# Performance work log

Measured on AMD Instinct MI355X. Metric: run time of the kernel, lower is better.

The kernel has to match this reference:

```python
import jax, jax.numpy as jnp
import numpy as np

N = 100000        # nodes in the batched graph
E = 1_600_000     # directed edges
G = 256           # graphs in the batch
IN, H = 3, 64
EPS = 1e-5        # BatchNorm eps (eval mode: running stats, dropout off)


def setup_inputs() -> dict:
    key = jax.random.key(0)
    ks = jax.random.split(key, 40)
    inp = {}
    inp["x"] = jax.random.normal(ks[0], (N, IN), jnp.float32)
    inp["edge_index"] = jax.random.randint(ks[1], (2, E), 0, N, dtype=jnp.int32)
    inp["batch_idx"] = jnp.sort(jax.random.randint(ks[2], (N,), 0, G, dtype=jnp.int32))
    dims = [IN, H, H, H]  # zip(dims[:-1], dims[1:]) -> 3 GCN layers (as in source)
    k = 3
    for i in range(3):
        inp[f"W{i}"] = jax.random.normal(ks[k], (dims[i], dims[i + 1]), jnp.float32) * 0.1; k += 1
        inp[f"b{i}"] = jax.random.normal(ks[k], (dims[i + 1],), jnp.float32) * 0.01; k += 1
        inp[f"g{i}"] = jax.random.uniform(ks[k], (dims[i + 1],), jnp.float32, 0.5, 1.5); k += 1
        inp[f"be{i}"] = jax.random.normal(ks[k], (dims[i + 1],), jnp.float32) * 0.1; k += 1
        inp[f"rm{i}"] = jax.random.normal(ks[k], (dims[i + 1],), jnp.float32) * 0.1; k += 1
        inp[f"rv{i}"] = jax.random.uniform(ks[k], (dims[i + 1],), jnp.float32, 0.5, 1.5); k += 1
    inp["mW1"] = jax.random.normal(ks[k], (2 * H, 32), jnp.float32) * 0.1; k += 1
    inp["mb1"] = jnp.zeros((32,), jnp.float32)
    inp["mW2"] = jax.random.normal(ks[k], (32, 16), jnp.float32) * 0.1; k += 1
    inp["mb2"] = jnp.zeros((16,), jnp.float32)
    inp["mW3"] = jax.random.normal(ks[k], (16, 1), jnp.float32) * 0.1; k += 1
    inp["mb3"] = jnp.zeros((1,), jnp.float32)
    return inp


def _gcn(x, W, b, src, dst):
    # PyG GCNConv: add self-loops, symmetric D^-1/2 (A+I) D^-1/2 normalization
    h = x @ W                                   # [N, out]
    deg = jnp.zeros((N,), h.dtype).at[dst].add(1.0) + 1.0  # +1 self-loop
    dinv = jax.lax.rsqrt(deg)
    coef = dinv[src] * dinv[dst]                # [E]
    agg = jax.ops.segment_sum(h[src] * coef[:, None], dst, num_segments=N)
    agg = agg + h * (dinv * dinv)[:, None]      # self-loop message
    return agg + b


def _bn(x, g, be, rm, rv):
    return (x - rm) * jax.lax.rsqrt(rv + EPS) * g + be


def _forward(x, edge_index, batch_idx,
             W0, b0, g0, be0, rm0, rv0,
             W1, b1, g1, be1, rm1, rv1,
             W2, b2, g2, be2, rm2, rv2,
             mW1, mb1, mW2, mb2, mW3, mb3):
    src, dst = edge_index[0], edge_index[1]
    layers = [(W0, b0, g0, be0, rm0, rv0), (W1, b1, g1, be1, rm1, rv1), (W2, b2, g2, be2, rm2, rv2)]
    for (W, b, g, be, rm, rv) in layers:
        x = jax.nn.relu(_bn(_gcn(x, W, b, src, dst), g, be, rm, rv))
    cnt = jax.ops.segment_sum(jnp.ones((N,), x.dtype), batch_idx, num_segments=G)
    x_mean = jax.ops.segment_sum(x, batch_idx, num_segments=G) / jnp.maximum(cnt, 1.0)[:, None]
    x_max = jax.ops.segment_max(x, batch_idx, num_segments=G)
    x_max = jnp.where(jnp.isfinite(x_max), x_max, 0.0)
    xg = jnp.concatenate([x_mean, x_max], axis=1)  # [G, 2H]
    h = jax.nn.relu(xg @ mW1 + mb1)
    h = jax.nn.relu(h @ mW2 + mb2)
    return h @ mW3 + mb3                            # [G, 1]


def reference(x, edge_index, batch_idx,
              W0, b0, g0, be0, rm0, rv0,
              W1, b1, g1, be1, rm1, rv1,
              W2, b2, g2, be2, rm2, rv2,
              mW1, mb1, mW2, mb2, mW3, mb3):
    return _forward(x, edge_index, batch_idx,
                    W0, b0, g0, be0, rm0, rv0,
                    W1, b1, g1, be1, rm1, rv1,
                    W2, b2, g2, be2, rm2, rv2,
                    mW1, mb1, mW2, mb2, mW3, mb3)
```

## Files before the change

### kernel.cpp

```cpp
#include <hip/hip_runtime.h>
#include <hip/hip_fp16.h>

#define NN 100000
#define EE 1600000
#define GG 256
#define EPS 1e-5f
#define KB2 ((NN + 511) >> 9)
#define EPB 4096
#define EBLK ((EE + EPB - 1) / EPB)
#define NB256 ((NN + 255) / 256)

__device__ __forceinline__ unsigned int pack2(float x, float y) {
  __half2 h = __float22half2_rn(make_float2(x, y));
  return *reinterpret_cast<unsigned int*>(&h);
}
__device__ __forceinline__ uint2 pack4(float x, float y, float z, float w) {
  uint2 r;
  r.x = pack2(x, y);
  r.y = pack2(z, w);
  return r;
}
__device__ __forceinline__ void add4(float4& a, uint2 v) {
  __half2 h0 = *reinterpret_cast<__half2*>(&v.x);
  __half2 h1 = *reinterpret_cast<__half2*>(&v.y);
  float2 f0 = __half22float2(h0);
  float2 f1 = __half22float2(h1);
  a.x += f0.x; a.y += f0.y; a.z += f1.x; a.w += f1.y;
}

__global__ void k_bcnt(const int* __restrict__ ei, int* __restrict__ bcnt) {
  __shared__ int cnt[KB2];
  int t = threadIdx.x;
  for (int i = t; i < KB2; i += 256) cnt[i] = 0;
  __syncthreads();
  int e0 = blockIdx.x * EPB;
#pragma unroll
  for (int j = 0; j < 16; ++j) {
    int e = e0 + j * 256 + t;
    if (e < EE) atomicAdd(&cnt[ei[EE + e] >> 9], 1);
  }
  __syncthreads();
  for (int i = t; i < KB2; i += 256)
    if (cnt[i] > 0) atomicAdd(&bcnt[i], cnt[i]);
}

__global__ void k_bscan(const int* __restrict__ bcnt, int* __restrict__ bbase,
                        int* __restrict__ bfill, int* __restrict__ row) {
  __shared__ int s[256];
  int t = threadIdx.x;
  int v = (t < KB2) ? bcnt[t] : 0;
  s[t] = v;
  __syncthreads();
  for (int off = 1; off < 256; off <<= 1) {
    int add = (t >= off) ? s[t - off] : 0;
    __syncthreads();
    s[t] += add;
    __syncthreads();
  }
  if (t < KB2) {
    int e = s[t] - v;
    bbase[t] = e;
    bfill[t] = e;
  }
  if (t == 0) {
    bbase[KB2] = EE;
    row[NN] = EE;
  }
}

__global__ void k_passA(const int* __restrict__ ei, int* __restrict__ bfill,
                        int2* __restrict__ tmp) {
  __shared__ int cnt[KB2], cur[KB2], base[KB2];
  int t = threadIdx.x;
  for (int b = t; b < KB2; b += 256) { cnt[b] = 0; cur[b] = 0; }
  __syncthreads();
  int e0 = blockIdx.x * EPB;
  int myb[16];
#pragma unroll
  for (int j = 0; j < 16; ++j) {
    int e = e0 + j * 256 + t;
    int bb = -1;
    if (e < EE) bb = ei[EE + e] >> 9;
    myb[j] = bb;
    if (bb >= 0) atomicAdd(&cnt[bb], 1);
  }
  __syncthreads();
  for (int b = t; b < KB2; b += 256)
    if (cnt[b] > 0) base[b] = atomicAdd(&bfill[b], cnt[b]);
  __syncthreads();
#pragma unroll
  for (int j = 0; j < 16; ++j) {
    int e = e0 + j * 256 + t;
    int bb = myb[j];
    if (bb >= 0) {
      int slot = base[bb] + atomicAdd(&cur[bb], 1);
      tmp[slot] = make_int2(ei[e], ei[EE + e]);
    }
  }
}

__global__ void k_bucket(const int2* __restrict__ tmp, const int* __restrict__ bbase,
                         const float* __restrict__ x, int* __restrict__ csr,
                         int* __restrict__ row, float* __restrict__ dinv,
                         float4* __restrict__ xd) {
  __shared__ int cnt[512], s[512], fillp[512];
  int b = blockIdx.x, t = threadIdx.x;
  int nb = b << 9;
  int e0 = bbase[b], e1 = bbase[b + 1];
  cnt[t] = 0;
  cnt[t + 256] = 0;
  __syncthreads();
  for (int e = e0 + t; e < e1; e += 256) atomicAdd(&cnt[tmp[e].y & 511], 1);
  __syncthreads();
  s[t] = cnt[t];
  s[t + 256] = cnt[t + 256];
  __syncthreads();
  for (int off = 1; off < 512; off <<= 1) {
    int i1 = t + 256;
    int v0 = (t >= off) ? s[t - off] : 0;
    int v1 = (i1 >= off) ? s[i1 - off] : 0;
    __syncthreads();
    s[t] += v0;
    s[i1] += v1;
    __syncthreads();
  }
#pragma unroll
  for (int k = 0; k < 2; ++k) {
    int i = t + k * 256;
    int excl = s[i] - cnt[i];
    fillp[i] = excl;
    int dst = nb + i;
    if (dst < NN) {
      row[dst] = e0 + excl;
      float d = rsqrtf((float)cnt[i] + 1.0f);
      dinv[dst] = d;
      xd[dst] = make_float4(x[dst * 3] * d, x[dst * 3 + 1] * d, x[dst * 3 + 2] * d, 0.f);
    }
  }
  __syncthreads();
  for (int e = e0 + t; e < e1; e += 256) {
    int2 ed = tmp[e];
    int slot = atomicAdd(&fillp[ed.y & 511], 1);
    csr[e0 + slot] = ed.x;
  }
}

__global__ void k_agg3f(const float4* __restrict__ xd, const int* __restrict__ row,
                        const int* __restrict__ csr, const float* __restrict__ dinv,
                        const float* __restrict__ W, const float* __restrict__ b,
                        const float* __restrict__ gam, const float* __restrict__ bet,
                        const float* __restrict__ rm, const float* __restrict__ rv,
                        uint2* __restrict__ out) {
  int n = blockIdx.x * 256 + threadIdx.x;
  if (n >= NN) return;
  int s0 = row[n], s1 = row[n + 1];
  float4 a = xd[n];
  float ax = a.x, ay = a.y, az = a.z;
  for (int i = s0; i < s1; i += 16) {
    int rem = s1 - i;
    int idx[16];
#pragma unroll
    for (int j = 0; j < 16; ++j) idx[j] = csr[min(i + j, s1 - 1)];
    float4 v[16];
#pragma unroll
    for (int j = 0; j < 16; ++j) v[j] = xd[idx[j]];
#pragma unroll
    for (int j = 0; j < 16; ++j)
      if (j < rem) { ax += v[j].x; ay += v[j].y; az += v[j].z; }
  }
  float d = dinv[n];
  float t0 = ax * d, t1 = ay * d, t2 = az * d;
  const float4* W4 = (const float4*)W;
  const float4* b4 = (const float4*)b;
  const float4* g4p = (const float4*)gam;
  const float4* be4p = (const float4*)bet;
  const float4* rm4p = (const float4*)rm;
  const float4* rv4p = (const float4*)rv;
#pragma unroll
  for (int c4 = 0; c4 < 16; ++c4) {
    float4 w0 = W4[c4], w1 = W4[16 + c4], w2 = W4[32 + c4];
    float4 bb = b4[c4], g4 = g4p[c4], be4 = be4p[c4], rm4 = rm4p[c4], rv4 = rv4p[c4];
    float4 o;
    o.x = fmaf(t0, w0.x, fmaf(t1, w1.x, fmaf(t2, w2.x, bb.x)));
    o.y = fmaf(t0, w0.y, fmaf(t1, w1.y, fmaf(t2, w2.y, bb.y)));
    o.z = fmaf(t0, w0.z, fmaf(t1, w1.z, fmaf(t2, w2.z, bb.z)));
    o.w = fmaf(t0, w0.w, fmaf(t1, w1.w, fmaf(t2, w2.w, bb.w)));
    float scx = g4.x * rsqrtf(rv4.x + EPS), shx = be4.x - rm4.x * scx;
    float scy = g4.y * rsqrtf(rv4.y + EPS), shy = be4.y - rm4.y * scy;
    float scz = g4.z * rsqrtf(rv4.z + EPS), shz = be4.z - rm4.z * scz;
    float scw = g4.w * rsqrtf(rv4.w + EPS), shw = be4.w - rm4.w * scw;
    o.x = fmaxf(fmaf(o.x, scx, shx), 0.f) * d;
    o.y = fmaxf(fmaf(o.y, scy, shy), 0.f) * d;
    o.z = fmaxf(fmaf(o.z, scz, shz), 0.f) * d;
    o.w = fmaxf(fmaf(o.w, scw, shw), 0.f) * d;
    out[(size_t)n * 16 + c4] = pack4(o.x, o.y, o.z, o.w);
  }
}

template <bool MID>
__global__ void k_layer2(const uint2* __restrict__ xs, const int* __restrict__ row,
                         const int* __restrict__ csr, const float* __restrict__ dinv,
                         const float* __restrict__ W, const float* __restrict__ b,
                         const float* __restrict__ gam, const float* __restrict__ bet,
                         const float* __restrict__ rm, const float* __restrict__ rv,
                         void* __restrict__ outv) {
  __shared__ float sh[16][68];
  int t = blockIdx.x * 256 + threadIdx.x;
  int n = t >> 4, sub = t & 15;
  int local = threadIdx.x >> 4;
  if (n >= NN) return;
  int s0 = row[n], s1 = row[n + 1];
  float4 a = make_float4(0.f, 0.f, 0.f, 0.f);
  add4(a, xs[(size_t)n * 16 + sub]);
  if (s0 < s1) {
    int e = s0 + sub;
    int myidx = (e < s1) ? csr[e] : n;
    for (int i = s0; i < s1; i += 16) {
      int e2 = i + 16 + sub;
      int pre = csr[min(e2, s1 - 1)];
      int nidx = (e2 < s1) ? pre : n;
      int rem = s1 - i;
      uint2 v[16];
#pragma unroll
      for (int j = 0; j < 16; ++j) {
        int idx = __shfl(myidx, j, 16);
        v[j] = xs[(size_t)idx * 16 + sub];
      }
#pragma unroll
      for (int j = 0; j < 16; ++j)
        if (j < rem) add4(a, v[j]);
      myidx = nidx;
    }
  }
  float d = dinv[n];
  sh[local][sub * 4 + 0] = a.x * d;
  sh[local][sub * 4 + 1] = a.y * d;
  sh[local][sub * 4 + 2] = a.z * d;
  sh[local][sub * 4 + 3] = a.w * d;
  __syncthreads();
  const float4* W4 = (const float4*)W;
  float4 acc = ((const float4*)b)[sub];
#pragma unroll 8
  for (int k = 0; k < 64; ++k) {
    float xv = sh[local][k];
    float4 w = W4[k * 16 + sub];
    acc.x = fmaf(xv, w.x, acc.x);
    acc.y = fmaf(xv, w.y, acc.y);
    acc.z = fmaf(xv, w.z, acc.z);
    acc.w = fmaf(xv, w.w, acc.w);
  }
  float4 g4 = ((const float4*)gam)[sub];
  float4 be4 = ((const float4*)bet)[sub];
  float4 rm4 = ((const float4*)rm)[sub];
  float4 rv4 = ((const float4*)rv)[sub];
  float scx = g4.x * rsqrtf(rv4.x + EPS), shx = be4.x - rm4.x * scx;
  float scy = g4.y * rsqrtf(rv4.y + EPS), shy = be4.y - rm4.y * scy;
  float scz = g4.z * rsqrtf(rv4.z + EPS), shz = be4.z - rm4.z * scz;
  float scw = g4.w * rsqrtf(rv4.w + EPS), shw = be4.w - rm4.w * scw;
  float4 o;
  o.x = fmaxf(fmaf(acc.x, scx, shx), 0.f);
  o.y = fmaxf(fmaf(acc.y, scy, shy), 0.f);
  o.z = fmaxf(fmaf(acc.z, scz, shz), 0.f);
  o.w = fmaxf(fmaf(acc.w, scw, shw), 0.f);
  if (MID) {
    ((uint2*)outv)[(size_t)n * 16 + sub] = pack4(o.x * d, o.y * d, o.z * d, o.w * d);
  } else {
    ((float4*)outv)[(size_t)n * 16 + sub] = o;
  }
}

__device__ __forceinline__ int lower_bound(const int* __restrict__ b, int target) {
  int lo = 0, hi = NN;
  while (lo < hi) {
    int m = (lo + hi) >> 1;
    if (b[m] < target) lo = m + 1; else hi = m;
  }
  return lo;
}

__global__ void k_poolmlp(const float* __restrict__ feat, const int* __restrict__ bidx,
                          const float* __restrict__ mW1, const float* __restrict__ mb1,
                          const float* __restrict__ mW2, const float* __restrict__ mb2,
                          const float* __restrict__ mW3, const float* __restrict__ mb3,
                          float* __restrict__ out) {
  __shared__ float ssum[4][64], smax[4][64], xg[128], h1[32], h2[16];
  int g = blockIdx.x, t = threadIdx.x;
  int c = t & 63, q = t >> 6;
  int lo = lower_bound(bidx, g);
  int hi = lower_bound(bidx, g + 1);
  float s = 0.f, m = 0.f;
  for (int i = lo + q; i < hi; i += 4) {
    float v = feat[(size_t)i * 64 + c];
    s += v;
    m = fmaxf(m, v);
  }
  ssum[q][c] = s;
  smax[q][c] = m;
  __syncthreads();
  if (q == 0) {
    float cs = ssum[0][c] + ssum[1][c] + ssum[2][c] + ssum[3][c];
    float cm = fmaxf(fmaxf(smax[0][c], smax[1][c]), fmaxf(smax[2][c], smax[3][c]));
    float cnt = fmaxf((float)(hi - lo), 1.0f);
    xg[c] = cs / cnt;
    xg[64 + c] = cm;
  }
  __syncthreads();
  if (t < 32) {
    float a = mb1[t];
    for (int k = 0; k < 128; ++k) a = fmaf(xg[k], mW1[k * 32 + t], a);
    h1[t] = fmaxf(a, 0.f);
  }
  __syncthreads();
  if (t < 16) {
    float a = mb2[t];
    for (int k = 0; k < 32; ++k) a = fmaf(h1[k], mW2[k * 16 + t], a);
    h2[t] = fmaxf(a, 0.f);
  }
  __syncthreads();
  if (t == 0) {
    float a = mb3[0];
    for (int k = 0; k < 16; ++k) a = fmaf(h2[k], mW3[k], a);
    out[g] = a;
  }
}

extern "C" void kernel_launch(void* const* d_in, const int* in_sizes, int n_in,
                              void* d_out, int out_size, void* d_ws, size_t ws_size,
                              hipStream_t stream) {
  const float* x = (const float*)d_in[0];
  const int* ei = (const int*)d_in[1];
  const int* bidx = (const int*)d_in[2];
  const float *W[3], *b[3], *gam[3], *bet[3], *rm[3], *rv[3];
  for (int l = 0; l < 3; ++l) {
    W[l] = (const float*)d_in[3 + 6 * l];
    b[l] = (const float*)d_in[4 + 6 * l];
    gam[l] = (const float*)d_in[5 + 6 * l];
    bet[l] = (const float*)d_in[6 + 6 * l];
    rm[l] = (const float*)d_in[7 + 6 * l];
    rv[l] = (const float*)d_in[8 + 6 * l];
  }
  const float* mW1 = (const float*)d_in[21];
  const float* mb1 = (const float*)d_in[22];
  const float* mW2 = (const float*)d_in[23];
  const float* mb2 = (const float*)d_in[24];
  const float* mW3 = (const float*)d_in[25];
  const float* mb3 = (const float*)d_in[26];
  float* out = (float*)d_out;

  char* ws = (char*)d_ws;
  size_t off = 0;
  auto alloc = [&](size_t bytes) {
    void* p = ws + off;
    off = (off + bytes + 1023) & ~(size_t)1023;
    return p;
  };
  float* dinv = (float*)alloc(NN * 4);
  int* row = (int*)alloc((NN + 1) * 4);
  int* csr = (int*)alloc((size_t)EE * 4);
  int* bcnt = (int*)alloc(256 * 4);
  int* bbase = (int*)alloc(256 * 4);
  int* bfill = (int*)alloc(256 * 4);
  float4* xd = (float4*)alloc((size_t)NN * 16);
  float* bufA = (float*)alloc((size_t)NN * 64 * 4);
  float* bufB = (float*)alloc((size_t)NN * 64 * 4);
  int2* tmp = (int2*)bufA;

  hipMemsetAsync(bcnt, 0, 256 * 4, stream);

  k_bcnt<<<EBLK, 256, 0, stream>>>(ei, bcnt);
  k_bscan<<<1, 256, 0, stream>>>(bcnt, bbase, bfill, row);
  k_passA<<<EBLK, 256, 0, stream>>>(ei, bfill, tmp);
  k_bucket<<<KB2, 256, 0, stream>>>(tmp, bbase, x, csr, row, dinv, xd);

  int nb16 = (NN * 16 + 255) / 256;

  k_agg3f<<<NB256, 256, 0, stream>>>(xd, row, csr, dinv, W[0], b[0], gam[0], bet[0],
                                     rm[0], rv[0], (uint2*)bufA);
  k_layer2<true><<<nb16, 256, 0, stream>>>((const uint2*)bufA, row, csr, dinv, W[1], b[1],
                                           gam[1], bet[1], rm[1], rv[1], (void*)bufB);
  k_layer2<false><<<nb16, 256, 0, stream>>>((const uint2*)bufB, row, csr, dinv, W[2], b[2],
                                            gam[2], bet[2], rm[2], rv[2], (void*)bufA);
  k_poolmlp<<<GG, 256, 0, stream>>>(bufA, bidx, mW1, mb1, mW2, mb2, mW3, mb3, out);
}
```

Before: 380.6 us.

## Pack edge temp to one int, double-buffer layer gathers, vectorize pooling

The bucketing temp array now stores each edge as a single int, holding the source shifted left by 9 bits plus the low 9 bits of the destination, instead of an int2. This halves that scratch traffic in passA and the bucket kernel; the packing only works because node ids fit in 23 bits. The layer2 gather loop is restructured to issue the next 16 neighbor loads before accumulating the current batch, which holds more loads in flight at the cost of registers. Pooling reads float4 per thread across 16 rows with a shared-memory reduction, replacing scalar loads over 4 rows.

```diff
diff --git a/kernel.cpp b/kernel.cpp
--- a/kernel.cpp
+++ b/kernel.cpp
@@ -69,7 +69,7 @@
 }
 
 __global__ void k_passA(const int* __restrict__ ei, int* __restrict__ bfill,
-                        int2* __restrict__ tmp) {
+                        int* __restrict__ tmp) {
   __shared__ int cnt[KB2], cur[KB2], base[KB2];
   int t = threadIdx.x;
   for (int b = t; b < KB2; b += 256) { cnt[b] = 0; cur[b] = 0; }
@@ -94,12 +94,12 @@
     int bb = myb[j];
     if (bb >= 0) {
       int slot = base[bb] + atomicAdd(&cur[bb], 1);
-      tmp[slot] = make_int2(ei[e], ei[EE + e]);
+      tmp[slot] = (ei[e] << 9) | (ei[EE + e] & 511);
     }
   }
 }
 
-__global__ void k_bucket(const int2* __restrict__ tmp, const int* __restrict__ bbase,
+__global__ void k_bucket(const int* __restrict__ tmp, const int* __restrict__ bbase,
                          const float* __restrict__ x, int* __restrict__ csr,
                          int* __restrict__ row, float* __restrict__ dinv,
                          float4* __restrict__ xd) {
@@ -110,7 +110,7 @@
   cnt[t] = 0;
   cnt[t + 256] = 0;
   __syncthreads();
-  for (int e = e0 + t; e < e1; e += 256) atomicAdd(&cnt[tmp[e].y & 511], 1);
+  for (int e = e0 + t; e < e1; e += 256) atomicAdd(&cnt[tmp[e] & 511], 1);
   __syncthreads();
   s[t] = cnt[t];
   s[t + 256] = cnt[t + 256];
@@ -139,9 +139,9 @@
   }
   __syncthreads();
   for (int e = e0 + t; e < e1; e += 256) {
-    int2 ed = tmp[e];
-    int slot = atomicAdd(&fillp[ed.y & 511], 1);
-    csr[e0 + slot] = ed.x;
+    int ed = tmp[e];
+    int slot = atomicAdd(&fillp[ed & 511], 1);
+    csr[e0 + slot] = ed >> 9;
   }
 }
 
@@ -213,23 +213,38 @@
   float4 a = make_float4(0.f, 0.f, 0.f, 0.f);
   add4(a, xs[(size_t)n * 16 + sub]);
   if (s0 < s1) {
-    int e = s0 + sub;
-    int myidx = (e < s1) ? csr[e] : n;
-    for (int i = s0; i < s1; i += 16) {
-      int e2 = i + 16 + sub;
-      int pre = csr[min(e2, s1 - 1)];
-      int nidx = (e2 < s1) ? pre : n;
-      int rem = s1 - i;
-      uint2 v[16];
-#pragma unroll
-      for (int j = 0; j < 16; ++j) {
-        int idx = __shfl(myidx, j, 16);
-        v[j] = xs[(size_t)idx * 16 + sub];
+    int pre0 = csr[min(s0 + sub, s1 - 1)];
+    int myidx = (s0 + sub < s1) ? pre0 : n;
+    uint2 vA[16];
+#pragma unroll
+    for (int j = 0; j < 16; ++j) {
+      int idx = __shfl(myidx, j, 16);
+      vA[j] = xs[(size_t)idx * 16 + sub];
+    }
+    int i = s0;
+    while (true) {
+      int inext = i + 16;
+      if (inext < s1) {
+        int pre = csr[min(inext + sub, s1 - 1)];
+        int nidx = (inext + sub < s1) ? pre : n;
+        uint2 vB[16];
+#pragma unroll
+        for (int j = 0; j < 16; ++j) {
+          int idx = __shfl(nidx, j, 16);
+          vB[j] = xs[(size_t)idx * 16 + sub];
+        }
+#pragma unroll
+        for (int j = 0; j < 16; ++j) add4(a, vA[j]);
+#pragma unroll
+        for (int j = 0; j < 16; ++j) vA[j] = vB[j];
+        i = inext;
+      } else {
+        int rem = s1 - i;
+#pragma unroll
+        for (int j = 0; j < 16; ++j)
+          if (j < rem) add4(a, vA[j]);
+        break;
       }
-#pragma unroll
-      for (int j = 0; j < 16; ++j)
-        if (j < rem) add4(a, v[j]);
-      myidx = nidx;
     }
   }
   float d = dinv[n];
@@ -278,31 +293,42 @@
   return lo;
 }
 
-__global__ void k_poolmlp(const float* __restrict__ feat, const int* __restrict__ bidx,
+__global__ void k_poolmlp(const float4* __restrict__ feat, const int* __restrict__ bidx,
                           const float* __restrict__ mW1, const float* __restrict__ mb1,
                           const float* __restrict__ mW2, const float* __restrict__ mb2,
                           const float* __restrict__ mW3, const float* __restrict__ mb3,
                           float* __restrict__ out) {
-  __shared__ float ssum[4][64], smax[4][64], xg[128], h1[32], h2[16];
+  __shared__ float4 shs[16][17], shm[16][17];
+  __shared__ float xg[128], h1[32], h2[16];
   int g = blockIdx.x, t = threadIdx.x;
-  int c = t & 63, q = t >> 6;
+  int c4 = t & 15, r = t >> 4;
   int lo = lower_bound(bidx, g);
   int hi = lower_bound(bidx, g + 1);
-  float s = 0.f, m = 0.f;
-  for (int i = lo + q; i < hi; i += 4) {
-    float v = feat[(size_t)i * 64 + c];
-    s += v;
-    m = fmaxf(m, v);
-  }
-  ssum[q][c] = s;
-  smax[q][c] = m;
-  __syncthreads();
-  if (q == 0) {
-    float cs = ssum[0][c] + ssum[1][c] + ssum[2][c] + ssum[3][c];
-    float cm = fmaxf(fmaxf(smax[0][c], smax[1][c]), fmaxf(smax[2][c], smax[3][c]));
-    float cnt = fmaxf((float)(hi - lo), 1.0f);
-    xg[c] = cs / cnt;
-    xg[64 + c] = cm;
+  float4 s = make_float4(0.f, 0.f, 0.f, 0.f);
+  float4 m = make_float4(0.f, 0.f, 0.f, 0.f);
+  for (int i = lo + r; i < hi; i += 16) {
+    float4 v = feat[(size_t)i * 16 + c4];
+    s.x += v.x; s.y += v.y; s.z += v.z; s.w += v.w;
+    m.x = fmaxf(m.x, v.x); m.y = fmaxf(m.y, v.y);
+    m.z = fmaxf(m.z, v.z); m.w = fmaxf(m.w, v.w);
+  }
+  shs[r][c4] = s;
+  shm[r][c4] = m;
+  __syncthreads();
+  if (t < 16) {
+    float4 cs = shs[0][t], cm = shm[0][t];
+#pragma unroll
+    for (int r2 = 1; r2 < 16; ++r2) {
+      float4 as = shs[r2][t], am = shm[r2][t];
+      cs.x += as.x; cs.y += as.y; cs.z += as.z; cs.w += as.w;
+      cm.x = fmaxf(cm.x, am.x); cm.y = fmaxf(cm.y, am.y);
+      cm.z = fmaxf(cm.z, am.z); cm.w = fmaxf(cm.w, am.w);
+    }
+    float inv = 1.0f / fmaxf((float)(hi - lo), 1.0f);
+    xg[t * 4 + 0] = cs.x * inv; xg[t * 4 + 1] = cs.y * inv;
+    xg[t * 4 + 2] = cs.z * inv; xg[t * 4 + 3] = cs.w * inv;
+    xg[64 + t * 4 + 0] = cm.x; xg[64 + t * 4 + 1] = cm.y;
+    xg[64 + t * 4 + 2] = cm.z; xg[64 + t * 4 + 3] = cm.w;
   }
   __syncthreads();
   if (t < 32) {
@@ -363,7 +389,7 @@
   float4* xd = (float4*)alloc((size_t)NN * 16);
   float* bufA = (float*)alloc((size_t)NN * 64 * 4);
   float* bufB = (float*)alloc((size_t)NN * 64 * 4);
-  int2* tmp = (int2*)bufA;
+  int* tmp = (int*)bufA;
 
   hipMemsetAsync(bcnt, 0, 256 * 4, stream);
 
@@ -380,5 +406,5 @@
                                            gam[1], bet[1], rm[1], rv[1], (void*)bufB);
   k_layer2<false><<<nb16, 256, 0, stream>>>((const uint2*)bufB, row, csr, dinv, W[2], b[2],
                                             gam[2], bet[2], rm[2], rv[2], (void*)bufA);
-  k_poolmlp<<<GG, 256, 0, stream>>>(bufA, bidx, mW1, mb1, mW2, mb2, mW3, mb3, out);
-}
+  k_poolmlp<<<GG, 256, 0, stream>>>((const float4*)bufA, bidx, mW1, mb1, mW2, mb2, mW3, mb3, out);
+}
```

Measured after the change: 362.5 us. 1.05x faster.
